# Optimization experiments

Measured on AMD Instinct MI355X. Metric: run time of the kernel, lower is better.

Reference implementation:

```python
import jax, jax.numpy as jnp
import numpy as np

N, DEG, FIN, HID, OUT = 50000, 16, 128, 128, 64


def setup_inputs() -> dict:
    key = jax.random.key(0)
    ks = jax.random.split(key, 32)
    x = jax.random.normal(ks[0], (N, FIN), dtype=jnp.float32)
    src = jax.random.randint(ks[1], (N * DEG,), 0, N, dtype=jnp.int32)
    dst = jnp.repeat(jnp.arange(N, dtype=jnp.int32), DEG)  # sorted by target, fixed degree
    edge_index = jnp.stack([src, dst])  # [2, E]
    dims = [(FIN, HID), (HID, HID), (HID, OUT)]
    params = {}
    i = 2
    for l, (fi, fo) in enumerate(dims, 1):
        s_lstm = 1.0 / np.sqrt(fi)
        params[f"W_ih{l}"] = jax.random.normal(ks[i + 0], (4 * fi, fi)) * s_lstm
        params[f"W_hh{l}"] = jax.random.normal(ks[i + 1], (4 * fi, fi)) * s_lstm
        params[f"b_ih{l}"] = jax.random.normal(ks[i + 2], (4 * fi,)) * s_lstm
        params[f"b_hh{l}"] = jax.random.normal(ks[i + 3], (4 * fi,)) * s_lstm
        params[f"Wl{l}"] = jax.random.normal(ks[i + 4], (fo, fi)) * (1.0 / np.sqrt(fi))
        params[f"bl{l}"] = jnp.zeros((fo,), jnp.float32)
        params[f"Wr{l}"] = jax.random.normal(ks[i + 5], (fo, fi)) * (1.0 / np.sqrt(fi))
        i += 6
    return {"x": x, "edge_index": edge_index, **params}


def _lstm_last(neigh, Wih, Whh, bih, bhh):
    # neigh: [N, deg, Fi]; PyTorch LSTM gate order i,f,g,o; return last-step output h.
    h0 = jnp.zeros((neigh.shape[0], Wih.shape[0] // 4), neigh.dtype)
    bias = bih + bhh

    def step(carry, xt):
        h, c = carry
        g = xt @ Wih.T + h @ Whh.T + bias
        i, f, gg, o = jnp.split(g, 4, axis=-1)
        c = jax.nn.sigmoid(f) * c + jax.nn.sigmoid(i) * jnp.tanh(gg)
        h = jax.nn.sigmoid(o) * jnp.tanh(c)
        return (h, c), None

    (h, _), _ = jax.lax.scan(step, (h0, h0), jnp.swapaxes(neigh, 0, 1))
    return h


def _sage_layer(x, src2d, Wih, Whh, bih, bhh, Wl, bl, Wr):
    neigh = x[src2d]  # gather: [N, deg, Fi]
    aggr = _lstm_last(neigh, Wih, Whh, bih, bhh)  # [N, Fi]
    return aggr @ Wl.T + bl + x @ Wr.T  # lin_l(aggr) + lin_r(x)


def reference(x, edge_index,
              W_ih1, W_hh1, b_ih1, b_hh1, Wl1, bl1, Wr1,
              W_ih2, W_hh2, b_ih2, b_hh2, Wl2, bl2, Wr2,
              W_ih3, W_hh3, b_ih3, b_hh3, Wl3, bl3, Wr3):
    n = x.shape[0]
    src2d = edge_index[0].reshape(n, -1)  # fixed-degree, dst-sorted edge list
    h = _sage_layer(x, src2d, W_ih1, W_hh1, b_ih1, b_hh1, Wl1, bl1, Wr1)
    h = jax.nn.relu(h)  # dropout is identity in eval mode
    h = _sage_layer(h, src2d, W_ih2, W_hh2, b_ih2, b_hh2, Wl2, bl2, Wr2)
    h = jax.nn.relu(h)
    return _sage_layer(h, src2d, W_ih3, W_hh3, b_ih3, b_hh3, Wl3, bl3, Wr3)
```

## Files before the change

### kernel.cpp

```cpp
#include <hip/hip_runtime.h>
#include <cstddef>
#include <cstdint>

typedef __attribute__((ext_vector_type(4))) float f32x4;
typedef __attribute__((ext_vector_type(8))) short short8;

#define HID 128
#define NK1 -1.4426950408889634f
#define PK2 2.8853900817779268f

#define BAR_LGKM() __asm__ volatile("s_waitcnt lgkmcnt(0)\ns_barrier" ::: "memory")
#define WAIT_VM2_BAR() __asm__ volatile("s_waitcnt vmcnt(2) lgkmcnt(0)\ns_barrier" ::: "memory")

__device__ __forceinline__ short f2bf(float f) {
  unsigned u = __builtin_bit_cast(unsigned, f);
  u += 0x7FFFu + ((u >> 16) & 1u);
  return (short)(u >> 16);
}
__device__ __forceinline__ unsigned pack_bf2(float a, float b) {
  unsigned ua = __builtin_bit_cast(unsigned, a) + 0x8000u;
  unsigned ub = __builtin_bit_cast(unsigned, b) + 0x8000u;
  return __builtin_amdgcn_perm(ub, ua, 0x07060302u);
}
__device__ __forceinline__ void unpack2(int w, float& lo, float& hi) {
  lo = __builtin_bit_cast(float, (unsigned)(w << 16));
  hi = __builtin_bit_cast(float, (unsigned)w & 0xffff0000u);
}

__device__ __forceinline__ float lstm_elem(float si, float sf, float sg, float so, float& c) {
  float Ei = __builtin_amdgcn_exp2f(si);
  float Ef = __builtin_amdgcn_exp2f(sf);
  float Tg = __builtin_amdgcn_exp2f(sg);
  float Eo = __builtin_amdgcn_exp2f(so);
  float u = 1.0f + Ei, w = 1.0f + Ef, v = Tg + 1.0f, Tm = Tg - 1.0f;
  float t0 = u * v;
  float num = __builtin_fmaf(c, t0, w * Tm);
  float cn = num * __builtin_amdgcn_rcpf(w * t0);
  c = cn;
  float Tc = __builtin_amdgcn_exp2f(PK2 * cn);
  return (Tc - 1.0f) * __builtin_amdgcn_rcpf((1.0f + Eo) * (Tc + 1.0f));
}

__global__ void conv_x_kernel(const float* __restrict__ x, short* __restrict__ xb, int n) {
  int i = blockIdx.x * blockDim.x + threadIdx.x;
  int stride = gridDim.x * blockDim.x;
  for (; i < n; i += stride) xb[i] = f2bf(x[i]);
}

__global__ void conv_layer_kernel(const float* __restrict__ Wih, const float* __restrict__ Whh,
                                  const float* __restrict__ bih, const float* __restrict__ bhh,
                                  const float* __restrict__ Wl, const float* __restrict__ Wr, int foK,
                                  short* __restrict__ wihB, short* __restrict__ whhB,
                                  short* __restrict__ wlB, short* __restrict__ wrB,
                                  float* __restrict__ bsum) {
  int i = blockIdx.x * blockDim.x + threadIdx.x;
  if (i < 512 * HID) {
    float sc = ((i >> 14) == 2) ? PK2 : NK1;
    wihB[i] = f2bf(Wih[i] * sc);
    whhB[i] = f2bf(Whh[i] * sc);
  }
  if (i < foK) { wlB[i] = f2bf(Wl[i]); wrB[i] = f2bf(Wr[i]); }
  if (i < 512) bsum[i] = (bih[i] + bhh[i]) * (((i >> 7) == 2) ? PK2 : NK1);
}

#define OSTR 524
__global__ __launch_bounds__(256, 2) void pgemm_kernel(
    const short* __restrict__ A, const short* __restrict__ W,
    const float* __restrict__ bias, short* __restrict__ out, int M, int ntiles) {
  __shared__ short ldsO[32 * OSTR];
  const int tid = threadIdx.x;
  const int wave = tid >> 6, lane = tid & 63;
  const int quad = lane >> 4, nn = lane & 15;

  short8 wreg[4][8];
#pragma unroll
  for (int kt = 0; kt < 4; ++kt)
#pragma unroll
    for (int nt = 0; nt < 8; ++nt)
      wreg[kt][nt] = *(const short8*)(W + (size_t)(wave * 128 + nt * 16 + nn) * HID + kt * 32 + quad * 8);
  f32x4 bias4[8];
#pragma unroll
  for (int nt = 0; nt < 8; ++nt)
#pragma unroll
    for (int r = 0; r < 4; ++r) bias4[nt][r] = bias[wave * 128 + nt * 16 + quad * 4 + r];

  const f32x4 zero4 = {0.f, 0.f, 0.f, 0.f};
#pragma unroll 1
  for (int rt = blockIdx.x; rt < ntiles; rt += gridDim.x) {
    const int row0 = rt * 32;
    f32x4 acc[2][8];
#pragma unroll
    for (int b = 0; b < 2; ++b)
#pragma unroll
      for (int nt = 0; nt < 8; ++nt) acc[b][nt] = zero4;
#pragma unroll
    for (int kt = 0; kt < 4; ++kt) {
      int r0 = row0 + nn;      if (r0 > M - 1) r0 = M - 1;
      int r1 = row0 + 16 + nn; if (r1 > M - 1) r1 = M - 1;
      short8 af0 = *(const short8*)(A + (size_t)r0 * HID + kt * 32 + quad * 8);
      short8 af1 = *(const short8*)(A + (size_t)r1 * HID + kt * 32 + quad * 8);
#pragma unroll
      for (int nt = 0; nt < 8; ++nt) {
        acc[0][nt] = __builtin_amdgcn_mfma_f32_16x16x32_bf16(wreg[kt][nt], af0, acc[0][nt], 0, 0, 0);
        acc[1][nt] = __builtin_amdgcn_mfma_f32_16x16x32_bf16(wreg[kt][nt], af1, acc[1][nt], 0, 0, 0);
      }
    }
    BAR_LGKM();
#pragma unroll
    for (int b = 0; b < 2; ++b)
#pragma unroll
      for (int nt = 0; nt < 8; ++nt) {
        f32x4 v = acc[b][nt] + bias4[nt];
        uint2 pk;
        pk.x = pack_bf2(v[0], v[1]);
        pk.y = pack_bf2(v[2], v[3]);
        *(uint2*)(ldsO + (b * 16 + nn) * OSTR + wave * 128 + nt * 16 + quad * 4) = pk;
      }
    BAR_LGKM();
#pragma unroll
    for (int idx = tid; idx < 32 * 64; idx += 256) {
      int row = idx >> 6, c8 = (idx & 63) * 8;
      if (row0 + row < M)
        *(short8*)(out + (size_t)(row0 + row) * 512 + c8) = *(const short8*)(ldsO + row * OSTR + c8);
    }
  }
}

template <int FO, bool RELU, bool OUTF32>
__global__ __launch_bounds__(256, 4) void outgemm_kernel(
    const short* __restrict__ A1, const short* __restrict__ W1,
    const short* __restrict__ A2, const short* __restrict__ W2,
    const float* __restrict__ bias,
    short* __restrict__ outB, float* __restrict__ outF, int M) {
  const int NTW = FO / 64;
  __shared__ char osm[8704];
  short* ldsO = (short*)osm;
  float* ldsF = (float*)osm;
  const int tid = threadIdx.x;
  const int wave = tid >> 6, lane = tid & 63;
  const int quad = lane >> 4, nn = lane & 15;
  const int cbase = wave * (FO / 4);
  const int row0 = blockIdx.x * 32;

  short8 w1r[4][NTW], w2r[4][NTW];
#pragma unroll
  for (int kt = 0; kt < 4; ++kt)
#pragma unroll
    for (int nt = 0; nt < NTW; ++nt) {
      w1r[kt][nt] = *(const short8*)(W1 + (size_t)(cbase + nt * 16 + nn) * HID + kt * 32 + quad * 8);
      w2r[kt][nt] = *(const short8*)(W2 + (size_t)(cbase + nt * 16 + nn) * HID + kt * 32 + quad * 8);
    }
  f32x4 bias4[NTW];
#pragma unroll
  for (int nt = 0; nt < NTW; ++nt)
#pragma unroll
    for (int r = 0; r < 4; ++r) bias4[nt][r] = bias[cbase + nt * 16 + quad * 4 + r];

  const f32x4 zero4 = {0.f, 0.f, 0.f, 0.f};
  f32x4 acc[2][NTW];
#pragma unroll
  for (int b = 0; b < 2; ++b)
#pragma unroll
    for (int nt = 0; nt < NTW; ++nt) acc[b][nt] = zero4;

#pragma unroll
  for (int kt = 0; kt < 4; ++kt) {
    int r0 = row0 + nn;      if (r0 > M - 1) r0 = M - 1;
    int r1 = row0 + 16 + nn; if (r1 > M - 1) r1 = M - 1;
    short8 a10 = *(const short8*)(A1 + (size_t)r0 * HID + kt * 32 + quad * 8);
    short8 a11 = *(const short8*)(A1 + (size_t)r1 * HID + kt * 32 + quad * 8);
    short8 a20 = *(const short8*)(A2 + (size_t)r0 * HID + kt * 32 + quad * 8);
    short8 a21 = *(const short8*)(A2 + (size_t)r1 * HID + kt * 32 + quad * 8);
#pragma unroll
    for (int nt = 0; nt < NTW; ++nt) {
      acc[0][nt] = __builtin_amdgcn_mfma_f32_16x16x32_bf16(w1r[kt][nt], a10, acc[0][nt], 0, 0, 0);
      acc[1][nt] = __builtin_amdgcn_mfma_f32_16x16x32_bf16(w1r[kt][nt], a11, acc[1][nt], 0, 0, 0);
      acc[0][nt] = __builtin_amdgcn_mfma_f32_16x16x32_bf16(w2r[kt][nt], a20, acc[0][nt], 0, 0, 0);
      acc[1][nt] = __builtin_amdgcn_mfma_f32_16x16x32_bf16(w2r[kt][nt], a21, acc[1][nt], 0, 0, 0);
    }
  }
#pragma unroll
  for (int b = 0; b < 2; ++b)
#pragma unroll
    for (int nt = 0; nt < NTW; ++nt) {
      f32x4 v = acc[b][nt] + bias4[nt];
      if (RELU) {
#pragma unroll
        for (int r = 0; r < 4; ++r) v[r] = fmaxf(v[r], 0.0f);
      }
      int lrow = b * 16 + nn;
      if (OUTF32) {
        *(f32x4*)(ldsF + lrow * 68 + cbase + nt * 16 + quad * 4) = v;
      } else {
        uint2 pk;
        pk.x = pack_bf2(v[0], v[1]);
        pk.y = pack_bf2(v[2], v[3]);
        *(uint2*)(ldsO + lrow * 136 + cbase + nt * 16 + quad * 4) = pk;
      }
    }
  BAR_LGKM();
  if (OUTF32) {
#pragma unroll
    for (int idx = tid; idx < 32 * 16; idx += 256) {
      int row = idx >> 4, c4 = (idx & 15) * 4;
      if (row0 + row < M)
        *(f32x4*)(outF + (size_t)(row0 + row) * 64 + c4) = *(const f32x4*)(ldsF + row * 68 + c4);
    }
  } else {
#pragma unroll
    for (int idx = tid; idx < 32 * 16; idx += 256) {
      int row = idx >> 4, c8 = (idx & 15) * 8;
      if (row0 + row < M)
        *(short8*)(outB + (size_t)(row0 + row) * 128 + c8) = *(const short8*)(ldsO + row * 136 + c8);
    }
  }
}

#define NPB 16
#define PSTR 520
#define HSTR 136
#define LSTM_LDS_BYTES ((2 * NPB * PSTR + 2 * NPB * HSTR) * 2 + 256 * 4)

__global__ __launch_bounds__(512, 4) void lstm_steps_kernel(
    const short* __restrict__ P, const short* __restrict__ Whh,
    const int* __restrict__ src, short* __restrict__ aggr, int M) {
  extern __shared__ char smem[];
  short* Pb = (short*)smem;
  short* Hb = Pb + 2 * NPB * PSTR;
  int* srcL = (int*)(Hb + 2 * NPB * HSTR);

  const int tid = threadIdx.x;
  const int wave = tid >> 6, lane = tid & 63;
  const int quad = lane >> 4, nn = lane & 15;
  const int nodeBase = blockIdx.x * NPB;
  const int r0row = wave * 2, r1row = wave * 2 + 1;

  short8 wreg[4][4];
#pragma unroll
  for (int kt = 0; kt < 4; ++kt)
#pragma unroll
    for (int q = 0; q < 4; ++q)
      wreg[kt][q] = *(const short8*)(Whh + (size_t)(q * 128 + wave * 16 + nn) * HID + kt * 32 + quad * 8);

  if (tid < 256) {
    int node = nodeBase + (tid >> 4);
    srcL[tid] = (node < M) ? src[nodeBase * 16 + tid] : 0;
  }

  float c_st[4] = {0.f, 0.f, 0.f, 0.f};

  __syncthreads();

  int sA = srcL[r0row * 16 + 0], sB = srcL[r1row * 16 + 0];
  __builtin_amdgcn_global_load_lds(
      (const __attribute__((address_space(1))) unsigned int*)(P + (size_t)sA * 512 + lane * 8),
      (__attribute__((address_space(3))) unsigned int*)(Pb + r0row * PSTR), 16, 0, 0);
  __builtin_amdgcn_global_load_lds(
      (const __attribute__((address_space(1))) unsigned int*)(P + (size_t)sB * 512 + lane * 8),
      (__attribute__((address_space(3))) unsigned int*)(Pb + r1row * PSTR), 16, 0, 0);
  sA = srcL[r0row * 16 + 1];
  sB = srcL[r1row * 16 + 1];

  const f32x4 zero4 = {0.f, 0.f, 0.f, 0.f};

#pragma unroll 1
  for (int t = 0; t < 16; ++t) {
    short* Pc = Pb + (t & 1) * NPB * PSTR;
    short* Pn = Pb + ((t + 1) & 1) * NPB * PSTR;
    short* Hp = Hb + ((t + 1) & 1) * NPB * HSTR;
    short* Hw = Hb + (t & 1) * NPB * HSTR;

    __builtin_amdgcn_global_load_lds(
        (const __attribute__((address_space(1))) unsigned int*)(P + (size_t)sA * 512 + lane * 8),
        (__attribute__((address_space(3))) unsigned int*)(Pn + r0row * PSTR), 16, 0, 0);
    __builtin_amdgcn_global_load_lds(
        (const __attribute__((address_space(1))) unsigned int*)(P + (size_t)sB * 512 + lane * 8),
        (__attribute__((address_space(3))) unsigned int*)(Pn + r1row * PSTR), 16, 0, 0);

    f32x4 acc[4];
#pragma unroll
    for (int q = 0; q < 4; ++q) acc[q] = zero4;
    if (t) {
#pragma unroll
      for (int kt = 0; kt < 4; ++kt) {
        short8 hb = *(const short8*)(Hp + nn * HSTR + kt * 32 + quad * 8);
#pragma unroll
        for (int q = 0; q < 4; ++q)
          acc[q] = __builtin_amdgcn_mfma_f32_16x16x32_bf16(wreg[kt][q], hb, acc[q], 0, 0, 0);
      }
    }

    WAIT_VM2_BAR();

    const short* pR = Pc + nn * PSTR + wave * 16 + quad * 4;
    uint2 p0 = *(const uint2*)(pR + 0 * 128);
    uint2 p1 = *(const uint2*)(pR + 1 * 128);
    uint2 p2 = *(const uint2*)(pR + 2 * 128);
    uint2 p3 = *(const uint2*)(pR + 3 * 128);
    float s0[4], s1[4], s2[4], s3[4];
    unpack2(p0.x, s0[0], s0[1]); unpack2(p0.y, s0[2], s0[3]);
    unpack2(p1.x, s1[0], s1[1]); unpack2(p1.y, s1[2], s1[3]);
    unpack2(p2.x, s2[0], s2[1]); unpack2(p2.y, s2[2], s2[3]);
    unpack2(p3.x, s3[0], s3[1]); unpack2(p3.y, s3[2], s3[3]);
    float hv[4];
#pragma unroll
    for (int r = 0; r < 4; ++r)
      hv[r] = lstm_elem(acc[0][r] + s0[r], acc[1][r] + s1[r],
                        acc[2][r] + s2[r], acc[3][r] + s3[r], c_st[r]);
    uint2 pk;
    pk.x = pack_bf2(hv[0], hv[1]);
    pk.y = pack_bf2(hv[2], hv[3]);
    *(uint2*)(Hw + nn * HSTR + wave * 16 + quad * 4) = pk;

    int tn = (t + 2 < 16) ? t + 2 : 15;
    sA = srcL[r0row * 16 + tn];
    sB = srcL[r1row * 16 + tn];

    BAR_LGKM();
  }

  if (tid < 256) {
    int rrow = tid >> 4, off = (tid & 15) * 8;
    int node = nodeBase + rrow;
    if (node < M)
      *(short8*)(aggr + (size_t)node * HID + off) = *(const short8*)(Hb + NPB * HSTR + rrow * HSTR + off);
  }
}

extern "C" void kernel_launch(void* const* d_in, const int* in_sizes, int n_in,
                              void* d_out, int out_size, void* d_ws, size_t ws_size,
                              hipStream_t stream) {
  const float* x = (const float*)d_in[0];
  const int* src = (const int*)d_in[1];
  const float* Wih[3] = {(const float*)d_in[2], (const float*)d_in[9], (const float*)d_in[16]};
  const float* Whh[3] = {(const float*)d_in[3], (const float*)d_in[10], (const float*)d_in[17]};
  const float* bih[3] = {(const float*)d_in[4], (const float*)d_in[11], (const float*)d_in[18]};
  const float* bhh[3] = {(const float*)d_in[5], (const float*)d_in[12], (const float*)d_in[19]};
  const float* Wl[3]  = {(const float*)d_in[6], (const float*)d_in[13], (const float*)d_in[20]};
  const float* bl[3]  = {(const float*)d_in[7], (const float*)d_in[14], (const float*)d_in[21]};
  const float* Wr[3]  = {(const float*)d_in[8], (const float*)d_in[15], (const float*)d_in[22]};

  const int M = in_sizes[0] / HID;

  char* ws = (char*)d_ws;
  size_t off = 0;
  auto alloc = [&](size_t bytes) -> void* {
    void* p = ws + off;
    off += (bytes + 255) & ~(size_t)255;
    return p;
  };
  short* curA = (short*)alloc((size_t)M * HID * 2);
  short* curB = (short*)alloc((size_t)M * HID * 2);
  short* aggr = (short*)alloc((size_t)M * HID * 2);
  short* Pbuf = (short*)alloc((size_t)M * 512 * 2);
  short* wihB[3]; short* whhB[3]; short* wlB[3]; short* wrB[3]; float* bsum[3];
  for (int l = 0; l < 3; ++l) {
    wihB[l] = (short*)alloc(512 * HID * 2);
    whhB[l] = (short*)alloc(512 * HID * 2);
    wlB[l]  = (short*)alloc(HID * HID * 2);
    wrB[l]  = (short*)alloc(HID * HID * 2);
    bsum[l] = (float*)alloc(512 * 4);
  }

  const int nblk = (M + NPB - 1) / NPB;
  const int ntiles = (M + 31) / 32;

  (void)hipFuncSetAttribute((const void*)lstm_steps_kernel,
                            hipFuncAttributeMaxDynamicSharedMemorySize, LSTM_LDS_BYTES);

  conv_x_kernel<<<2048, 256, 0, stream>>>(x, curA, M * HID);
  for (int l = 0; l < 3; ++l) {
    const int Fo = (l == 2) ? 64 : 128;
    conv_layer_kernel<<<256, 256, 0, stream>>>(Wih[l], Whh[l], bih[l], bhh[l], Wl[l], Wr[l],
                                               Fo * HID, wihB[l], whhB[l], wlB[l], wrB[l], bsum[l]);
  }

  short* cur = curA;
  short* nxt = curB;
  for (int l = 0; l < 3; ++l) {
    pgemm_kernel<<<512, 256, 0, stream>>>(cur, wihB[l], bsum[l], Pbuf, M, ntiles);
    lstm_steps_kernel<<<nblk, 512, LSTM_LDS_BYTES, stream>>>(Pbuf, whhB[l], src, aggr, M);
    if (l < 2) {
      outgemm_kernel<128, true, false><<<ntiles, 256, 0, stream>>>(
          aggr, wlB[l], cur, wrB[l], bl[l], nxt, nullptr, M);
      short* tswap = cur; cur = nxt; nxt = tswap;
    } else {
      outgemm_kernel<64, false, true><<<ntiles, 256, 0, stream>>>(
          aggr, wlB[l], cur, wrB[l], bl[l], nullptr, (float*)d_out, M);
    }
  }
}
```

Before: 867.3 us.

## Persist LSTM blocks over node tiles, widen pgemm to 8 waves, fold bias into accumulators

The LSTM step kernel becomes persistent: 512 blocks loop over node tiles and reuse the recurrent weights already held in registers. Each step now waits for all outstanding loads at one barrier, seeds the MFMA accumulators with the gathered input projection, and only then issues the next step's prefetch. This removes the separate add and the partial vmcnt wait, at the cost of less overlap between the prefetch and the step's compute. pgemm moves to 512 threads, with each wave covering 64 columns and the bias used as the initial accumulator; outgemm also initialises its accumulators from the bias. The H LDS stride changes from 136 to 152, probably to alter bank mapping.

```diff
diff --git a/kernel.cpp b/kernel.cpp
--- a/kernel.cpp
+++ b/kernel.cpp
@@ -10,7 +10,7 @@
 #define PK2 2.8853900817779268f
 
 #define BAR_LGKM() __asm__ volatile("s_waitcnt lgkmcnt(0)\ns_barrier" ::: "memory")
-#define WAIT_VM2_BAR() __asm__ volatile("s_waitcnt vmcnt(2) lgkmcnt(0)\ns_barrier" ::: "memory")
+#define STEP_BAR() __asm__ volatile("s_waitcnt vmcnt(0) lgkmcnt(0)\ns_barrier" ::: "memory")
 
 __device__ __forceinline__ short f2bf(float f) {
   unsigned u = __builtin_bit_cast(unsigned, f);
@@ -25,6 +25,12 @@
 __device__ __forceinline__ void unpack2(int w, float& lo, float& hi) {
   lo = __builtin_bit_cast(float, (unsigned)(w << 16));
   hi = __builtin_bit_cast(float, (unsigned)w & 0xffff0000u);
+}
+__device__ __forceinline__ float2 unpack2v(int w) {
+  float2 r;
+  r.x = __builtin_bit_cast(float, (unsigned)(w << 16));
+  r.y = __builtin_bit_cast(float, (unsigned)w & 0xffff0000u);
+  return r;
 }
 
 __device__ __forceinline__ float lstm_elem(float si, float sf, float sg, float so, float& c) {
@@ -64,35 +70,35 @@
 }
 
 #define OSTR 524
-__global__ __launch_bounds__(256, 2) void pgemm_kernel(
+__global__ __launch_bounds__(512, 4) void pgemm_kernel(
     const short* __restrict__ A, const short* __restrict__ W,
     const float* __restrict__ bias, short* __restrict__ out, int M, int ntiles) {
   __shared__ short ldsO[32 * OSTR];
   const int tid = threadIdx.x;
   const int wave = tid >> 6, lane = tid & 63;
   const int quad = lane >> 4, nn = lane & 15;
-
-  short8 wreg[4][8];
+  const int cbase = wave * 64;
+
+  short8 wreg[4][4];
 #pragma unroll
   for (int kt = 0; kt < 4; ++kt)
 #pragma unroll
-    for (int nt = 0; nt < 8; ++nt)
-      wreg[kt][nt] = *(const short8*)(W + (size_t)(wave * 128 + nt * 16 + nn) * HID + kt * 32 + quad * 8);
-  f32x4 bias4[8];
-#pragma unroll
-  for (int nt = 0; nt < 8; ++nt)
-#pragma unroll
-    for (int r = 0; r < 4; ++r) bias4[nt][r] = bias[wave * 128 + nt * 16 + quad * 4 + r];
-
-  const f32x4 zero4 = {0.f, 0.f, 0.f, 0.f};
+    for (int nt = 0; nt < 4; ++nt)
+      wreg[kt][nt] = *(const short8*)(W + (size_t)(cbase + nt * 16 + nn) * HID + kt * 32 + quad * 8);
+  f32x4 bias4[4];
+#pragma unroll
+  for (int nt = 0; nt < 4; ++nt)
+#pragma unroll
+    for (int r = 0; r < 4; ++r) bias4[nt][r] = bias[cbase + nt * 16 + quad * 4 + r];
+
 #pragma unroll 1
   for (int rt = blockIdx.x; rt < ntiles; rt += gridDim.x) {
     const int row0 = rt * 32;
-    f32x4 acc[2][8];
+    f32x4 acc[2][4];
 #pragma unroll
     for (int b = 0; b < 2; ++b)
 #pragma unroll
-      for (int nt = 0; nt < 8; ++nt) acc[b][nt] = zero4;
+      for (int nt = 0; nt < 4; ++nt) acc[b][nt] = bias4[nt];
 #pragma unroll
     for (int kt = 0; kt < 4; ++kt) {
       int r0 = row0 + nn;      if (r0 > M - 1) r0 = M - 1;
@@ -100,7 +106,7 @@
       short8 af0 = *(const short8*)(A + (size_t)r0 * HID + kt * 32 + quad * 8);
       short8 af1 = *(const short8*)(A + (size_t)r1 * HID + kt * 32 + quad * 8);
 #pragma unroll
-      for (int nt = 0; nt < 8; ++nt) {
+      for (int nt = 0; nt < 4; ++nt) {
         acc[0][nt] = __builtin_amdgcn_mfma_f32_16x16x32_bf16(wreg[kt][nt], af0, acc[0][nt], 0, 0, 0);
         acc[1][nt] = __builtin_amdgcn_mfma_f32_16x16x32_bf16(wreg[kt][nt], af1, acc[1][nt], 0, 0, 0);
       }
@@ -109,16 +115,15 @@
 #pragma unroll
     for (int b = 0; b < 2; ++b)
 #pragma unroll
-      for (int nt = 0; nt < 8; ++nt) {
-        f32x4 v = acc[b][nt] + bias4[nt];
+      for (int nt = 0; nt < 4; ++nt) {
         uint2 pk;
-        pk.x = pack_bf2(v[0], v[1]);
-        pk.y = pack_bf2(v[2], v[3]);
-        *(uint2*)(ldsO + (b * 16 + nn) * OSTR + wave * 128 + nt * 16 + quad * 4) = pk;
+        pk.x = pack_bf2(acc[b][nt][0], acc[b][nt][1]);
+        pk.y = pack_bf2(acc[b][nt][2], acc[b][nt][3]);
+        *(uint2*)(ldsO + (b * 16 + nn) * OSTR + cbase + nt * 16 + quad * 4) = pk;
       }
     BAR_LGKM();
 #pragma unroll
-    for (int idx = tid; idx < 32 * 64; idx += 256) {
+    for (int idx = tid; idx < 32 * 64; idx += 512) {
       int row = idx >> 6, c8 = (idx & 63) * 8;
       if (row0 + row < M)
         *(short8*)(out + (size_t)(row0 + row) * 512 + c8) = *(const short8*)(ldsO + row * OSTR + c8);
@@ -150,18 +155,13 @@
       w1r[kt][nt] = *(const short8*)(W1 + (size_t)(cbase + nt * 16 + nn) * HID + kt * 32 + quad * 8);
       w2r[kt][nt] = *(const short8*)(W2 + (size_t)(cbase + nt * 16 + nn) * HID + kt * 32 + quad * 8);
     }
-  f32x4 bias4[NTW];
-#pragma unroll
-  for (int nt = 0; nt < NTW; ++nt)
-#pragma unroll
-    for (int r = 0; r < 4; ++r) bias4[nt][r] = bias[cbase + nt * 16 + quad * 4 + r];
-
-  const f32x4 zero4 = {0.f, 0.f, 0.f, 0.f};
   f32x4 acc[2][NTW];
 #pragma unroll
   for (int b = 0; b < 2; ++b)
 #pragma unroll
-    for (int nt = 0; nt < NTW; ++nt) acc[b][nt] = zero4;
+    for (int nt = 0; nt < NTW; ++nt)
+#pragma unroll
+      for (int r = 0; r < 4; ++r) acc[b][nt][r] = bias[cbase + nt * 16 + quad * 4 + r];
 
 #pragma unroll
   for (int kt = 0; kt < 4; ++kt) {
@@ -183,7 +183,7 @@
   for (int b = 0; b < 2; ++b)
 #pragma unroll
     for (int nt = 0; nt < NTW; ++nt) {
-      f32x4 v = acc[b][nt] + bias4[nt];
+      f32x4 v = acc[b][nt];
       if (RELU) {
 #pragma unroll
         for (int r = 0; r < 4; ++r) v[r] = fmaxf(v[r], 0.0f);
@@ -218,12 +218,12 @@
 
 #define NPB 16
 #define PSTR 520
-#define HSTR 136
+#define HSTR 152
 #define LSTM_LDS_BYTES ((2 * NPB * PSTR + 2 * NPB * HSTR) * 2 + 256 * 4)
 
 __global__ __launch_bounds__(512, 4) void lstm_steps_kernel(
     const short* __restrict__ P, const short* __restrict__ Whh,
-    const int* __restrict__ src, short* __restrict__ aggr, int M) {
+    const int* __restrict__ src, short* __restrict__ aggr, int M, int ntiles) {
   extern __shared__ char smem[];
   short* Pb = (short*)smem;
   short* Hb = Pb + 2 * NPB * PSTR;
@@ -232,7 +232,6 @@
   const int tid = threadIdx.x;
   const int wave = tid >> 6, lane = tid & 63;
   const int quad = lane >> 4, nn = lane & 15;
-  const int nodeBase = blockIdx.x * NPB;
   const int r0row = wave * 2, r1row = wave * 2 + 1;
 
   short8 wreg[4][4];
@@ -242,88 +241,91 @@
     for (int q = 0; q < 4; ++q)
       wreg[kt][q] = *(const short8*)(Whh + (size_t)(q * 128 + wave * 16 + nn) * HID + kt * 32 + quad * 8);
 
-  if (tid < 256) {
-    int node = nodeBase + (tid >> 4);
-    srcL[tid] = (node < M) ? src[nodeBase * 16 + tid] : 0;
-  }
-
-  float c_st[4] = {0.f, 0.f, 0.f, 0.f};
-
-  __syncthreads();
-
-  int sA = srcL[r0row * 16 + 0], sB = srcL[r1row * 16 + 0];
-  __builtin_amdgcn_global_load_lds(
-      (const __attribute__((address_space(1))) unsigned int*)(P + (size_t)sA * 512 + lane * 8),
-      (__attribute__((address_space(3))) unsigned int*)(Pb + r0row * PSTR), 16, 0, 0);
-  __builtin_amdgcn_global_load_lds(
-      (const __attribute__((address_space(1))) unsigned int*)(P + (size_t)sB * 512 + lane * 8),
-      (__attribute__((address_space(3))) unsigned int*)(Pb + r1row * PSTR), 16, 0, 0);
-  sA = srcL[r0row * 16 + 1];
-  sB = srcL[r1row * 16 + 1];
-
-  const f32x4 zero4 = {0.f, 0.f, 0.f, 0.f};
-
 #pragma unroll 1
-  for (int t = 0; t < 16; ++t) {
-    short* Pc = Pb + (t & 1) * NPB * PSTR;
-    short* Pn = Pb + ((t + 1) & 1) * NPB * PSTR;
-    short* Hp = Hb + ((t + 1) & 1) * NPB * HSTR;
-    short* Hw = Hb + (t & 1) * NPB * HSTR;
-
+  for (int tile = blockIdx.x; tile < ntiles; tile += gridDim.x) {
+    const int nodeBase = tile * NPB;
+    if (tid < 256) {
+      int node = nodeBase + (tid >> 4);
+      srcL[tid] = (node < M) ? src[nodeBase * 16 + tid] : 0;
+    }
+    float c_st[4] = {0.f, 0.f, 0.f, 0.f};
+    BAR_LGKM();
+
+    int sA = srcL[r0row * 16 + 0], sB = srcL[r1row * 16 + 0];
     __builtin_amdgcn_global_load_lds(
         (const __attribute__((address_space(1))) unsigned int*)(P + (size_t)sA * 512 + lane * 8),
-        (__attribute__((address_space(3))) unsigned int*)(Pn + r0row * PSTR), 16, 0, 0);
+        (__attribute__((address_space(3))) unsigned int*)(Pb + r0row * PSTR), 16, 0, 0);
     __builtin_amdgcn_global_load_lds(
         (const __attribute__((address_space(1))) unsigned int*)(P + (size_t)sB * 512 + lane * 8),
-        (__attribute__((address_space(3))) unsigned int*)(Pn + r1row * PSTR), 16, 0, 0);
-
-    f32x4 acc[4];
-#pragma unroll
-    for (int q = 0; q < 4; ++q) acc[q] = zero4;
-    if (t) {
-#pragma unroll
-      for (int kt = 0; kt < 4; ++kt) {
-        short8 hb = *(const short8*)(Hp + nn * HSTR + kt * 32 + quad * 8);
-#pragma unroll
-        for (int q = 0; q < 4; ++q)
-          acc[q] = __builtin_amdgcn_mfma_f32_16x16x32_bf16(wreg[kt][q], hb, acc[q], 0, 0, 0);
-      }
-    }
-
-    WAIT_VM2_BAR();
-
-    const short* pR = Pc + nn * PSTR + wave * 16 + quad * 4;
-    uint2 p0 = *(const uint2*)(pR + 0 * 128);
-    uint2 p1 = *(const uint2*)(pR + 1 * 128);
-    uint2 p2 = *(const uint2*)(pR + 2 * 128);
-    uint2 p3 = *(const uint2*)(pR + 3 * 128);
-    float s0[4], s1[4], s2[4], s3[4];
-    unpack2(p0.x, s0[0], s0[1]); unpack2(p0.y, s0[2], s0[3]);
-    unpack2(p1.x, s1[0], s1[1]); unpack2(p1.y, s1[2], s1[3]);
-    unpack2(p2.x, s2[0], s2[1]); unpack2(p2.y, s2[2], s2[3]);
-    unpack2(p3.x, s3[0], s3[1]); unpack2(p3.y, s3[2], s3[3]);
-    float hv[4];
-#pragma unroll
-    for (int r = 0; r < 4; ++r)
-      hv[r] = lstm_elem(acc[0][r] + s0[r], acc[1][r] + s1[r],
-                        acc[2][r] + s2[r], acc[3][r] + s3[r], c_st[r]);
-    uint2 pk;
-    pk.x = pack_bf2(hv[0], hv[1]);
-    pk.y = pack_bf2(hv[2], hv[3]);
-    *(uint2*)(Hw + nn * HSTR + wave * 16 + quad * 4) = pk;
-
-    int tn = (t + 2 < 16) ? t + 2 : 15;
-    sA = srcL[r0row * 16 + tn];
-    sB = srcL[r1row * 16 + tn];
+        (__attribute__((address_space(3))) unsigned int*)(Pb + r1row * PSTR), 16, 0, 0);
+    sA = srcL[r0row * 16 + 1];
+    sB = srcL[r1row * 16 + 1];
+
+#pragma unroll 1
+    for (int t = 0; t < 16; ++t) {
+      short* Pc = Pb + (t & 1) * NPB * PSTR;
+      short* Pn = Pb + ((t + 1) & 1) * NPB * PSTR;
+      const short* Hp = Hb + ((t + 1) & 1) * NPB * HSTR;
+      short* Hw = Hb + (t & 1) * NPB * HSTR;
+
+      STEP_BAR();
+
+      const short* pR = Pc + nn * PSTR + wave * 16 + quad * 4;
+      uint2 p0 = *(const uint2*)(pR + 0 * 128);
+      uint2 p1 = *(const uint2*)(pR + 1 * 128);
+      uint2 p2 = *(const uint2*)(pR + 2 * 128);
+      uint2 p3 = *(const uint2*)(pR + 3 * 128);
+      f32x4 acc[4];
+      {
+        float2 a0 = unpack2v(p0.x), a1 = unpack2v(p0.y);
+        acc[0][0] = a0.x; acc[0][1] = a0.y; acc[0][2] = a1.x; acc[0][3] = a1.y;
+        float2 b0 = unpack2v(p1.x), b1 = unpack2v(p1.y);
+        acc[1][0] = b0.x; acc[1][1] = b0.y; acc[1][2] = b1.x; acc[1][3] = b1.y;
+        float2 c0 = unpack2v(p2.x), c1 = unpack2v(p2.y);
+        acc[2][0] = c0.x; acc[2][1] = c0.y; acc[2][2] = c1.x; acc[2][3] = c1.y;
+        float2 d0 = unpack2v(p3.x), d1 = unpack2v(p3.y);
+        acc[3][0] = d0.x; acc[3][1] = d0.y; acc[3][2] = d1.x; acc[3][3] = d1.y;
+      }
+
+      if (t < 15) {
+        __builtin_amdgcn_global_load_lds(
+            (const __attribute__((address_space(1))) unsigned int*)(P + (size_t)sA * 512 + lane * 8),
+            (__attribute__((address_space(3))) unsigned int*)(Pn + r0row * PSTR), 16, 0, 0);
+        __builtin_amdgcn_global_load_lds(
+            (const __attribute__((address_space(1))) unsigned int*)(P + (size_t)sB * 512 + lane * 8),
+            (__attribute__((address_space(3))) unsigned int*)(Pn + r1row * PSTR), 16, 0, 0);
+        int tn = (t + 2 < 16) ? t + 2 : 15;
+        sA = srcL[r0row * 16 + tn];
+        sB = srcL[r1row * 16 + tn];
+      }
+
+      if (t) {
+#pragma unroll
+        for (int kt = 0; kt < 4; ++kt) {
+          short8 hb = *(const short8*)(Hp + nn * HSTR + kt * 32 + quad * 8);
+#pragma unroll
+          for (int q = 0; q < 4; ++q)
+            acc[q] = __builtin_amdgcn_mfma_f32_16x16x32_bf16(wreg[kt][q], hb, acc[q], 0, 0, 0);
+        }
+      }
+
+      float hv[4];
+#pragma unroll
+      for (int r = 0; r < 4; ++r)
+        hv[r] = lstm_elem(acc[0][r], acc[1][r], acc[2][r], acc[3][r], c_st[r]);
+      uint2 pk;
+      pk.x = pack_bf2(hv[0], hv[1]);
+      pk.y = pack_bf2(hv[2], hv[3]);
+      *(uint2*)(Hw + nn * HSTR + wave * 16 + quad * 4) = pk;
+    }
 
     BAR_LGKM();
-  }
-
-  if (tid < 256) {
-    int rrow = tid >> 4, off = (tid & 15) * 8;
-    int node = nodeBase + rrow;
-    if (node < M)
-      *(short8*)(aggr + (size_t)node * HID + off) = *(const short8*)(Hb + NPB * HSTR + rrow * HSTR + off);
+    if (tid < 256) {
+      int rrow = tid >> 4, off = (tid & 15) * 8;
+      int node = nodeBase + rrow;
+      if (node < M)
+        *(short8*)(aggr + (size_t)node * HID + off) = *(const short8*)(Hb + NPB * HSTR + rrow * HSTR + off);
+    }
   }
 }
 
@@ -362,7 +364,7 @@
     bsum[l] = (float*)alloc(512 * 4);
   }
 
-  const int nblk = (M + NPB - 1) / NPB;
+  const int nltiles = (M + NPB - 1) / NPB;
   const int ntiles = (M + 31) / 32;
 
   (void)hipFuncSetAttribute((const void*)lstm_steps_kernel,
@@ -378,8 +380,8 @@
   short* cur = curA;
   short* nxt = curB;
   for (int l = 0; l < 3; ++l) {
-    pgemm_kernel<<<512, 256, 0, stream>>>(cur, wihB[l], bsum[l], Pbuf, M, ntiles);
-    lstm_steps_kernel<<<nblk, 512, LSTM_LDS_BYTES, stream>>>(Pbuf, whhB[l], src, aggr, M);
+    pgemm_kernel<<<1024, 512, 0, stream>>>(cur, wihB[l], bsum[l], Pbuf, M, ntiles);
+    lstm_steps_kernel<<<512, 512, LSTM_LDS_BYTES, stream>>>(Pbuf, whhB[l], src, aggr, M, nltiles);
     if (l < 2) {
       outgemm_kernel<128, true, false><<<ntiles, 256, 0, stream>>>(
           aggr, wlB[l], cur, wrB[l], bl[l], nxt, nullptr, M);
```

Result: faster. 797.5 us (-8.0%).
